# Kernel optimization log

Hardware: AMD Instinct MI355X
Metric: run time of the kernel (lower is better)

Reference implementation:

```python
import jax, jax.numpy as jnp
import numpy as np

TEMPERATURE = 8.0  # sqrt(head_dim=64)
_MASKING_VALUE = -1e30  # float32 branch of the original module


def setup_inputs() -> dict:
    key = jax.random.key(0)
    kq, kk, kv = jax.random.split(key, 3)
    B, H, S, D = 2, 12, 2048, 64
    q = jax.random.normal(kq, (B, H, S, D), dtype=jnp.float32)
    k = jax.random.normal(kk, (B, H, S, D), dtype=jnp.float32)
    v = jax.random.normal(kv, (B, H, S, D), dtype=jnp.float32)
    # causal mask, broadcastable over batch and heads; mask==0 -> masked
    mask = jnp.tril(jnp.ones((S, S), dtype=jnp.bool_))[None, None, :, :]
    return {"q": q, "k": k, "v": v, "mask": mask}


def reference(q, k, v, mask):
    # attn = (q / temperature) @ k^T  -> [B,H,S,S]
    scores = jnp.einsum("bhqd,bhkd->bhqk", q / TEMPERATURE, k)
    scores = jnp.where(mask, scores, _MASKING_VALUE)
    attn = jax.nn.softmax(scores, axis=-1)  # dropout in eval mode (identity)
    output = jnp.einsum("bhqk,bhkd->bhqd", attn, v)
    return (output, attn)
```

## Files before the change

kernel.cpp:

```cpp
#include <hip/hip_runtime.h>
#include <hip/hip_bf16.h>
#include <stdint.h>

#define SS 2048
#define DD 64
#define NHEAD 24
#define TQ 64
#define TK 64
#define NKT 32

typedef __attribute__((ext_vector_type(8))) short short8;
typedef __attribute__((ext_vector_type(4))) short short4v;
typedef __attribute__((ext_vector_type(4))) float f32x4;

#define QSCALE 0.18033688011112042f
#define MLOG   46.166241308446828f

#if __has_builtin(__builtin_amdgcn_exp2f)
#define EXP2(x) __builtin_amdgcn_exp2f(x)
#else
#define EXP2(x) exp2f(x)
#endif

__device__ __forceinline__ unsigned short f2bf(float x) {
  union { float f; unsigned u; } a; a.f = x;
  unsigned r = a.u + 0x7FFFu + ((a.u >> 16) & 1u);
  return (unsigned short)(r >> 16);
}
__device__ __forceinline__ float bf2f(unsigned short u) {
  union { unsigned u; float f; } a; a.u = ((unsigned)u) << 16;
  return a.f;
}

__device__ __forceinline__ void stage16(const unsigned char* g, unsigned char* l) {
  __builtin_amdgcn_global_load_lds(
      (const __attribute__((address_space(1))) unsigned int*)g,
      (__attribute__((address_space(3))) unsigned int*)l, 16, 0, 0);
}

__global__ __launch_bounds__(256) void prep_kernel(
    const float* __restrict__ q, const float* __restrict__ k,
    const float* __restrict__ v, unsigned short* __restrict__ qb,
    unsigned char* __restrict__ kb, unsigned char* __restrict__ vtb) {
  const int head = blockIdx.x >> 5;
  const int t64 = blockIdx.x & 31;
  const int tid = threadIdx.x;
  const int c4 = tid & 15;
  const size_t inbase = ((size_t)head * SS + (size_t)t64 * 64) * DD;
  const f32x4* qsrc = (const f32x4*)(q + inbase);
  const f32x4* ksrc = (const f32x4*)(k + inbase);
  const f32x4* vsrc = (const f32x4*)(v + inbase);
  unsigned short* qdst = qb + inbase;
  unsigned char* ktile = kb + ((size_t)(head * NKT + t64) << 13);
  unsigned char* vtile = vtb + ((size_t)(head * NKT + t64) << 13);
#pragma unroll
  for (int j = 0; j < 4; ++j) {
    const int row = (tid >> 4) + 16 * j;
    f32x4 xq = qsrc[row * 16 + c4];
    short4v hq;
    hq.x = (short)f2bf(xq.x * QSCALE); hq.y = (short)f2bf(xq.y * QSCALE);
    hq.z = (short)f2bf(xq.z * QSCALE); hq.w = (short)f2bf(xq.w * QSCALE);
    *(short4v*)(qdst + row * 64 + c4 * 4) = hq;

    f32x4 xk = ksrc[row * 16 + c4];
    short4v hk;
    hk.x = (short)f2bf(xk.x); hk.y = (short)f2bf(xk.y);
    hk.z = (short)f2bf(xk.z); hk.w = (short)f2bf(xk.w);
    const int chunk = c4 >> 1, half = c4 & 1;
    *(short4v*)(ktile + row * 128 + ((chunk ^ (row & 7)) << 4) + half * 8) = hk;

    f32x4 xv = vsrc[row * 16 + c4];
    float vals[4] = {xv.x, xv.y, xv.z, xv.w};
#pragma unroll
    for (int e = 0; e < 4; ++e) {
      const int d = c4 * 4 + e;
      *(unsigned short*)(vtile + d * 128 + (((row >> 3) ^ (d & 7)) << 4) +
                         (row & 7) * 2) = f2bf(vals[e]);
    }
  }
}

__global__ __launch_bounds__(256) void sdpa_kernel(
    const unsigned short* __restrict__ qb, const unsigned char* __restrict__ kb,
    const unsigned char* __restrict__ vtb, float* __restrict__ out,
    float* __restrict__ attn) {
  __shared__ unsigned char lds[40960];

  const int bid = blockIdx.x;
  const int xcd = bid & 7;
  const int seq = bid >> 3;
  const int head = xcd * 3 + (seq >> 5);
  const int qt = seq & 31;
  const int q0 = qt * TQ;

  const int tid = threadIdx.x;
  const int w = tid >> 6;
  const int l = tid & 63;
  const int lhi = l >> 4;
  const int llo = l & 15;

  const unsigned short* qh = qb + (size_t)head * SS * DD;
  const unsigned char* kh = kb + ((size_t)(head * NKT) << 13);
  const unsigned char* vh = vtb + ((size_t)(head * NKT) << 13);
  float* oh = out + (size_t)head * SS * DD;
  float* ah = attn + (size_t)head * SS * SS;

  unsigned char* ldsP = lds + 32768;

  const int qrow_a = q0 + 16 * w + llo;
  short8 qf0 = *(const short8*)(qh + (size_t)qrow_a * DD + lhi * 8);
  short8 qf1 = *(const short8*)(qh + (size_t)qrow_a * DD + lhi * 8 + 32);

  float lsum[4] = {0.f, 0.f, 0.f, 0.f};

  int b = 0;
  stage16(kh + tid * 16, lds + tid * 16);
  stage16(kh + 4096 + tid * 16, lds + 4096 + tid * 16);
  __syncthreads();
  for (int kt = 0; kt <= qt; ++kt) {
    if (kt < qt) {
      const unsigned char* src = kh + ((size_t)(kt + 1) << 13);
      unsigned char* dst = lds + (b ^ 1) * 8192;
      stage16(src + tid * 16, dst + tid * 16);
      stage16(src + 4096 + tid * 16, dst + 4096 + tid * 16);
    }
    const unsigned char* kbuf = lds + b * 8192;
    f32x4 s[4];
#pragma unroll
    for (int c = 0; c < 4; ++c) {
      const int br = 16 * c + llo;
      short8 kf0 = *(const short8*)(kbuf + br * 128 + ((lhi ^ (br & 7)) << 4));
      short8 kf1 = *(const short8*)(kbuf + br * 128 + (((lhi + 4) ^ (br & 7)) << 4));
      f32x4 acc = {0.f, 0.f, 0.f, 0.f};
      acc = __builtin_amdgcn_mfma_f32_16x16x32_bf16(qf0, kf0, acc, 0, 0, 0);
      acc = __builtin_amdgcn_mfma_f32_16x16x32_bf16(qf1, kf1, acc, 0, 0, 0);
      s[c] = acc;
    }
    if (kt == qt) {
#pragma unroll
      for (int c = 0; c < 4; ++c)
#pragma unroll
        for (int r = 0; r < 4; ++r) {
          int qrow = 16 * w + 4 * lhi + r;
          int kcol = 16 * c + llo;
          if (kcol > qrow) s[c][r] = -INFINITY;
        }
    }
#pragma unroll
    for (int c = 0; c < 4; ++c)
#pragma unroll
      for (int r = 0; r < 4; ++r) lsum[r] += EXP2(s[c][r] - MLOG);
    __syncthreads();
    b ^= 1;
  }

  float linv[4];
#pragma unroll
  for (int r = 0; r < 4; ++r) {
    float ps = lsum[r];
    ps += __shfl_xor(ps, 1);
    ps += __shfl_xor(ps, 2);
    ps += __shfl_xor(ps, 4);
    ps += __shfl_xor(ps, 8);
    linv[r] = 1.0f / ps;
  }

  f32x4 o[4];
#pragma unroll
  for (int c = 0; c < 4; ++c) o[c] = (f32x4){0.f, 0.f, 0.f, 0.f};

  b = 0;
  stage16(kh + tid * 16, lds + tid * 16);
  stage16(kh + 4096 + tid * 16, lds + 4096 + tid * 16);
  stage16(vh + tid * 16, lds + 16384 + tid * 16);
  stage16(vh + 4096 + tid * 16, lds + 16384 + 4096 + tid * 16);
  __syncthreads();
  for (int kt = 0; kt <= qt; ++kt) {
    if (kt < qt) {
      const unsigned char* ksrc = kh + ((size_t)(kt + 1) << 13);
      const unsigned char* vsrc = vh + ((size_t)(kt + 1) << 13);
      unsigned char* kdst = lds + (b ^ 1) * 8192;
      unsigned char* vdst = lds + 16384 + (b ^ 1) * 8192;
      stage16(ksrc + tid * 16, kdst + tid * 16);
      stage16(ksrc + 4096 + tid * 16, kdst + 4096 + tid * 16);
      stage16(vsrc + tid * 16, vdst + tid * 16);
      stage16(vsrc + 4096 + tid * 16, vdst + 4096 + tid * 16);
    }
    const unsigned char* kbuf = lds + b * 8192;
    const unsigned char* vbuf = lds + 16384 + b * 8192;

    f32x4 s[4];
#pragma unroll
    for (int c = 0; c < 4; ++c) {
      const int br = 16 * c + llo;
      short8 kf0 = *(const short8*)(kbuf + br * 128 + ((lhi ^ (br & 7)) << 4));
      short8 kf1 = *(const short8*)(kbuf + br * 128 + (((lhi + 4) ^ (br & 7)) << 4));
      f32x4 acc = {0.f, 0.f, 0.f, 0.f};
      acc = __builtin_amdgcn_mfma_f32_16x16x32_bf16(qf0, kf0, acc, 0, 0, 0);
      acc = __builtin_amdgcn_mfma_f32_16x16x32_bf16(qf1, kf1, acc, 0, 0, 0);
      s[c] = acc;
    }
    if (kt == qt) {
#pragma unroll
      for (int c = 0; c < 4; ++c)
#pragma unroll
        for (int r = 0; r < 4; ++r) {
          int qrow = 16 * w + 4 * lhi + r;
          int kcol = 16 * c + llo;
          if (kcol > qrow) s[c][r] = -INFINITY;
        }
    }
#pragma unroll
    for (int c = 0; c < 4; ++c)
#pragma unroll
      for (int r = 0; r < 4; ++r) {
        float p = EXP2(s[c][r] - MLOG) * linv[r];
        const int qrow = 16 * w + 4 * lhi + r;
        const int kcol = 16 * c + llo;
        *(unsigned short*)(ldsP + qrow * 128 + (((kcol >> 3) ^ (qrow & 7)) << 4) +
                           (kcol & 7) * 2) = f2bf(p);
      }
    __syncthreads();

    const int k0 = kt * TK;
#pragma unroll
    for (int j = 0; j < 4; ++j) {
      const int row = (tid >> 4) + 16 * j;
      const int cg = tid & 15;
      short4v pv = *(const short4v*)(ldsP + row * 128 +
                                     (((cg >> 1) ^ (row & 7)) << 4) + (cg & 1) * 8);
      f32x4 fo;
      fo.x = bf2f((unsigned short)pv.x);
      fo.y = bf2f((unsigned short)pv.y);
      fo.z = bf2f((unsigned short)pv.z);
      fo.w = bf2f((unsigned short)pv.w);
      *(f32x4*)(ah + (size_t)(q0 + row) * SS + k0 + cg * 4) = fo;
    }

    {
      const int pr = 16 * w + llo;
      short8 pa0 = *(const short8*)(ldsP + pr * 128 + ((lhi ^ (pr & 7)) << 4));
      short8 pa1 = *(const short8*)(ldsP + pr * 128 + (((lhi + 4) ^ (pr & 7)) << 4));
#pragma unroll
      for (int c = 0; c < 4; ++c) {
        const int vr = 16 * c + llo;
        short8 vb0 = *(const short8*)(vbuf + vr * 128 + ((lhi ^ (vr & 7)) << 4));
        short8 vb1 = *(const short8*)(vbuf + vr * 128 + (((lhi + 4) ^ (vr & 7)) << 4));
        o[c] = __builtin_amdgcn_mfma_f32_16x16x32_bf16(pa0, vb0, o[c], 0, 0, 0);
        o[c] = __builtin_amdgcn_mfma_f32_16x16x32_bf16(pa1, vb1, o[c], 0, 0, 0);
      }
    }
    __syncthreads();
    b ^= 1;
  }

  {
    const int zc = (qt + 1) * TK;
#pragma unroll
    for (int j = 0; j < 4; ++j) {
      int row = q0 + 16 * w + 4 * j + lhi;
      f32x4* dst = (f32x4*)(ah + (size_t)row * SS);
      for (int c = (zc >> 2) + llo; c < (SS >> 2); c += 16)
        dst[c] = (f32x4){0.f, 0.f, 0.f, 0.f};
    }
  }

#pragma unroll
  for (int c = 0; c < 4; ++c)
#pragma unroll
    for (int r = 0; r < 4; ++r) {
      int qrow = q0 + 16 * w + 4 * lhi + r;
      oh[(size_t)qrow * DD + 16 * c + llo] = o[c][r];
    }
}

extern "C" void kernel_launch(void* const* d_in, const int* in_sizes, int n_in,
                              void* d_out, int out_size, void* d_ws, size_t ws_size,
                              hipStream_t stream) {
  const float* q = (const float*)d_in[0];
  const float* k = (const float*)d_in[1];
  const float* v = (const float*)d_in[2];
  float* out = (float*)d_out;
  float* attn = out + (size_t)NHEAD * SS * DD;

  const size_t QKV_BYTES = (size_t)NHEAD * SS * DD * 2;
  unsigned short* qb = (unsigned short*)d_ws;
  unsigned char* kb = (unsigned char*)d_ws + QKV_BYTES;
  unsigned char* vtb = kb + QKV_BYTES;

  prep_kernel<<<dim3(NHEAD * NKT), dim3(256), 0, stream>>>(q, k, v, qb, kb, vtb);
  sdpa_kernel<<<dim3(NHEAD * NKT), dim3(256), 0, stream>>>(qb, kb, vtb, out, attn);
}
```

Before: 481.0 us.

## Keep P in registers via transposed QK MFMA and bpermute instead of LDS round-trip

Computes S^T by swapping the MFMA operands, so each lane holds scores for one query row. The softmax row sum then needs only two cross-lane shuffles. P is packed to bf16 in registers and reshuffled into the A-operand layout with ds_bpermute, which removes the LDS P buffer and one __syncthreads per tile. Attention rows are written straight from registers with nontemporal stores, deferred by one iteration to overlap with compute. The cost is more VGPR pressure and bpermute traffic, plus stores that are less coalesced because each lane writes 16-byte chunks along its own row.

```diff
diff --git a/kernel.cpp b/kernel.cpp
--- a/kernel.cpp
+++ b/kernel.cpp
@@ -5,7 +5,6 @@
 #define SS 2048
 #define DD 64
 #define NHEAD 24
-#define TQ 64
 #define TK 64
 #define NKT 32
 
@@ -26,10 +25,6 @@
   union { float f; unsigned u; } a; a.f = x;
   unsigned r = a.u + 0x7FFFu + ((a.u >> 16) & 1u);
   return (unsigned short)(r >> 16);
-}
-__device__ __forceinline__ float bf2f(unsigned short u) {
-  union { unsigned u; float f; } a; a.u = ((unsigned)u) << 16;
-  return a.f;
 }
 
 __device__ __forceinline__ void stage16(const unsigned char* g, unsigned char* l) {
@@ -84,39 +79,37 @@
     const unsigned short* __restrict__ qb, const unsigned char* __restrict__ kb,
     const unsigned char* __restrict__ vtb, float* __restrict__ out,
     float* __restrict__ attn) {
-  __shared__ unsigned char lds[40960];
+  __shared__ unsigned char lds[32768];
 
   const int bid = blockIdx.x;
   const int xcd = bid & 7;
   const int seq = bid >> 3;
   const int head = xcd * 3 + (seq >> 5);
   const int qt = seq & 31;
-  const int q0 = qt * TQ;
+  const int q0 = qt * TK;
 
   const int tid = threadIdx.x;
   const int w = tid >> 6;
   const int l = tid & 63;
   const int lhi = l >> 4;
   const int llo = l & 15;
+  const int qrl = 16 * w + llo;
 
   const unsigned short* qh = qb + (size_t)head * SS * DD;
   const unsigned char* kh = kb + ((size_t)(head * NKT) << 13);
   const unsigned char* vh = vtb + ((size_t)(head * NKT) << 13);
   float* oh = out + (size_t)head * SS * DD;
   float* ah = attn + (size_t)head * SS * SS;
-
-  unsigned char* ldsP = lds + 32768;
-
-  const int qrow_a = q0 + 16 * w + llo;
-  short8 qf0 = *(const short8*)(qh + (size_t)qrow_a * DD + lhi * 8);
-  short8 qf1 = *(const short8*)(qh + (size_t)qrow_a * DD + lhi * 8 + 32);
-
-  float lsum[4] = {0.f, 0.f, 0.f, 0.f};
-
-  int b = 0;
+  float* ah_row = ah + (size_t)(q0 + qrl) * SS;
+
+  short8 qf0 = *(const short8*)(qh + (size_t)(q0 + qrl) * DD + lhi * 8);
+  short8 qf1 = *(const short8*)(qh + (size_t)(q0 + qrl) * DD + lhi * 8 + 32);
+
+  float lsum = 0.f;
   stage16(kh + tid * 16, lds + tid * 16);
   stage16(kh + 4096 + tid * 16, lds + 4096 + tid * 16);
   __syncthreads();
+  int b = 0;
   for (int kt = 0; kt <= qt; ++kt) {
     if (kt < qt) {
       const unsigned char* src = kh + ((size_t)(kt + 1) << 13);
@@ -125,49 +118,35 @@
       stage16(src + 4096 + tid * 16, dst + 4096 + tid * 16);
     }
     const unsigned char* kbuf = lds + b * 8192;
-    f32x4 s[4];
+    const bool diag = (kt == qt);
 #pragma unroll
     for (int c = 0; c < 4; ++c) {
       const int br = 16 * c + llo;
       short8 kf0 = *(const short8*)(kbuf + br * 128 + ((lhi ^ (br & 7)) << 4));
       short8 kf1 = *(const short8*)(kbuf + br * 128 + (((lhi + 4) ^ (br & 7)) << 4));
       f32x4 acc = {0.f, 0.f, 0.f, 0.f};
-      acc = __builtin_amdgcn_mfma_f32_16x16x32_bf16(qf0, kf0, acc, 0, 0, 0);
-      acc = __builtin_amdgcn_mfma_f32_16x16x32_bf16(qf1, kf1, acc, 0, 0, 0);
-      s[c] = acc;
-    }
-    if (kt == qt) {
-#pragma unroll
-      for (int c = 0; c < 4; ++c)
-#pragma unroll
-        for (int r = 0; r < 4; ++r) {
-          int qrow = 16 * w + 4 * lhi + r;
-          int kcol = 16 * c + llo;
-          if (kcol > qrow) s[c][r] = -INFINITY;
-        }
-    }
-#pragma unroll
-    for (int c = 0; c < 4; ++c)
-#pragma unroll
-      for (int r = 0; r < 4; ++r) lsum[r] += EXP2(s[c][r] - MLOG);
+      acc = __builtin_amdgcn_mfma_f32_16x16x32_bf16(kf0, qf0, acc, 0, 0, 0);
+      acc = __builtin_amdgcn_mfma_f32_16x16x32_bf16(kf1, qf1, acc, 0, 0, 0);
+#pragma unroll
+      for (int r = 0; r < 4; ++r) {
+        float sv = acc[r];
+        if (diag && (16 * c + 4 * lhi + r > qrl)) sv = -INFINITY;
+        lsum += EXP2(sv - MLOG);
+      }
+    }
     __syncthreads();
     b ^= 1;
   }
-
-  float linv[4];
-#pragma unroll
-  for (int r = 0; r < 4; ++r) {
-    float ps = lsum[r];
-    ps += __shfl_xor(ps, 1);
-    ps += __shfl_xor(ps, 2);
-    ps += __shfl_xor(ps, 4);
-    ps += __shfl_xor(ps, 8);
-    linv[r] = 1.0f / ps;
-  }
+  lsum += __shfl_xor(lsum, 16);
+  lsum += __shfl_xor(lsum, 32);
+  const float linv = 1.0f / lsum;
 
   f32x4 o[4];
 #pragma unroll
   for (int c = 0; c < 4; ++c) o[c] = (f32x4){0.f, 0.f, 0.f, 0.f};
+
+  unsigned sv[8];
+  int k0p = 0;
 
   b = 0;
   stage16(kh + tid * 16, lds + tid * 16);
@@ -175,7 +154,22 @@
   stage16(vh + tid * 16, lds + 16384 + tid * 16);
   stage16(vh + 4096 + tid * 16, lds + 16384 + 4096 + tid * 16);
   __syncthreads();
+
+  const int i0 = ((((2 * lhi)) & 3) * 16 + llo) * 4;
+  const int i1 = ((((2 * lhi) + 1) & 3) * 16 + llo) * 4;
+
   for (int kt = 0; kt <= qt; ++kt) {
+    if (kt > 0) {
+#pragma unroll
+      for (int c = 0; c < 4; ++c) {
+        f32x4 fo;
+        fo.x = __uint_as_float(sv[2 * c] << 16);
+        fo.y = __uint_as_float(sv[2 * c] & 0xFFFF0000u);
+        fo.z = __uint_as_float(sv[2 * c + 1] << 16);
+        fo.w = __uint_as_float(sv[2 * c + 1] & 0xFFFF0000u);
+        __builtin_nontemporal_store(fo, (f32x4*)(ah_row + k0p + 16 * c + 4 * lhi));
+      }
+    }
     if (kt < qt) {
       const unsigned char* ksrc = kh + ((size_t)(kt + 1) << 13);
       const unsigned char* vsrc = vh + ((size_t)(kt + 1) << 13);
@@ -188,70 +182,68 @@
     }
     const unsigned char* kbuf = lds + b * 8192;
     const unsigned char* vbuf = lds + 16384 + b * 8192;
-
-    f32x4 s[4];
+    const bool diag = (kt == qt);
+
+    unsigned pk[8];
 #pragma unroll
     for (int c = 0; c < 4; ++c) {
       const int br = 16 * c + llo;
       short8 kf0 = *(const short8*)(kbuf + br * 128 + ((lhi ^ (br & 7)) << 4));
       short8 kf1 = *(const short8*)(kbuf + br * 128 + (((lhi + 4) ^ (br & 7)) << 4));
       f32x4 acc = {0.f, 0.f, 0.f, 0.f};
-      acc = __builtin_amdgcn_mfma_f32_16x16x32_bf16(qf0, kf0, acc, 0, 0, 0);
-      acc = __builtin_amdgcn_mfma_f32_16x16x32_bf16(qf1, kf1, acc, 0, 0, 0);
-      s[c] = acc;
-    }
-    if (kt == qt) {
-#pragma unroll
-      for (int c = 0; c < 4; ++c)
-#pragma unroll
-        for (int r = 0; r < 4; ++r) {
-          int qrow = 16 * w + 4 * lhi + r;
-          int kcol = 16 * c + llo;
-          if (kcol > qrow) s[c][r] = -INFINITY;
-        }
-    }
-#pragma unroll
-    for (int c = 0; c < 4; ++c)
+      acc = __builtin_amdgcn_mfma_f32_16x16x32_bf16(kf0, qf0, acc, 0, 0, 0);
+      acc = __builtin_amdgcn_mfma_f32_16x16x32_bf16(kf1, qf1, acc, 0, 0, 0);
+      float p[4];
 #pragma unroll
       for (int r = 0; r < 4; ++r) {
-        float p = EXP2(s[c][r] - MLOG) * linv[r];
-        const int qrow = 16 * w + 4 * lhi + r;
-        const int kcol = 16 * c + llo;
-        *(unsigned short*)(ldsP + qrow * 128 + (((kcol >> 3) ^ (qrow & 7)) << 4) +
-                           (kcol & 7) * 2) = f2bf(p);
+        float s = acc[r];
+        if (diag && (16 * c + 4 * lhi + r > qrl)) s = -INFINITY;
+        p[r] = EXP2(s - MLOG) * linv;
       }
-    __syncthreads();
-
-    const int k0 = kt * TK;
-#pragma unroll
-    for (int j = 0; j < 4; ++j) {
-      const int row = (tid >> 4) + 16 * j;
-      const int cg = tid & 15;
-      short4v pv = *(const short4v*)(ldsP + row * 128 +
-                                     (((cg >> 1) ^ (row & 7)) << 4) + (cg & 1) * 8);
-      f32x4 fo;
-      fo.x = bf2f((unsigned short)pv.x);
-      fo.y = bf2f((unsigned short)pv.y);
-      fo.z = bf2f((unsigned short)pv.z);
-      fo.w = bf2f((unsigned short)pv.w);
-      *(f32x4*)(ah + (size_t)(q0 + row) * SS + k0 + cg * 4) = fo;
-    }
-
-    {
-      const int pr = 16 * w + llo;
-      short8 pa0 = *(const short8*)(ldsP + pr * 128 + ((lhi ^ (pr & 7)) << 4));
-      short8 pa1 = *(const short8*)(ldsP + pr * 128 + (((lhi + 4) ^ (pr & 7)) << 4));
-#pragma unroll
-      for (int c = 0; c < 4; ++c) {
-        const int vr = 16 * c + llo;
-        short8 vb0 = *(const short8*)(vbuf + vr * 128 + ((lhi ^ (vr & 7)) << 4));
-        short8 vb1 = *(const short8*)(vbuf + vr * 128 + (((lhi + 4) ^ (vr & 7)) << 4));
-        o[c] = __builtin_amdgcn_mfma_f32_16x16x32_bf16(pa0, vb0, o[c], 0, 0, 0);
-        o[c] = __builtin_amdgcn_mfma_f32_16x16x32_bf16(pa1, vb1, o[c], 0, 0, 0);
-      }
-    }
+      pk[2 * c] = ((unsigned)f2bf(p[1]) << 16) | f2bf(p[0]);
+      pk[2 * c + 1] = ((unsigned)f2bf(p[3]) << 16) | f2bf(p[2]);
+    }
+
+    union U { int i[4]; short8 v; } fa0, fa1;
+#pragma unroll
+    for (int jb = 0; jb < 2; ++jb) {
+      int a0 = __builtin_amdgcn_ds_bpermute(i0, (int)pk[0 + jb]);
+      int b0 = __builtin_amdgcn_ds_bpermute(i0, (int)pk[2 + jb]);
+      fa0.i[jb] = (lhi < 2) ? a0 : b0;
+      int a1 = __builtin_amdgcn_ds_bpermute(i1, (int)pk[0 + jb]);
+      int b1 = __builtin_amdgcn_ds_bpermute(i1, (int)pk[2 + jb]);
+      fa0.i[2 + jb] = (lhi < 2) ? a1 : b1;
+      int c0 = __builtin_amdgcn_ds_bpermute(i0, (int)pk[4 + jb]);
+      int d0 = __builtin_amdgcn_ds_bpermute(i0, (int)pk[6 + jb]);
+      fa1.i[jb] = (lhi < 2) ? c0 : d0;
+      int c1 = __builtin_amdgcn_ds_bpermute(i1, (int)pk[4 + jb]);
+      int d1 = __builtin_amdgcn_ds_bpermute(i1, (int)pk[6 + jb]);
+      fa1.i[2 + jb] = (lhi < 2) ? c1 : d1;
+    }
+
+#pragma unroll
+    for (int c = 0; c < 4; ++c) {
+      const int vr = 16 * c + llo;
+      short8 vb0 = *(const short8*)(vbuf + vr * 128 + ((lhi ^ (vr & 7)) << 4));
+      short8 vb1 = *(const short8*)(vbuf + vr * 128 + (((lhi + 4) ^ (vr & 7)) << 4));
+      o[c] = __builtin_amdgcn_mfma_f32_16x16x32_bf16(fa0.v, vb0, o[c], 0, 0, 0);
+      o[c] = __builtin_amdgcn_mfma_f32_16x16x32_bf16(fa1.v, vb1, o[c], 0, 0, 0);
+    }
+
+#pragma unroll
+    for (int t = 0; t < 8; ++t) sv[t] = pk[t];
+    k0p = kt * TK;
     __syncthreads();
     b ^= 1;
+  }
+#pragma unroll
+  for (int c = 0; c < 4; ++c) {
+    f32x4 fo;
+    fo.x = __uint_as_float(sv[2 * c] << 16);
+    fo.y = __uint_as_float(sv[2 * c] & 0xFFFF0000u);
+    fo.z = __uint_as_float(sv[2 * c + 1] << 16);
+    fo.w = __uint_as_float(sv[2 * c + 1] & 0xFFFF0000u);
+    __builtin_nontemporal_store(fo, (f32x4*)(ah_row + k0p + 16 * c + 4 * lhi));
   }
 
   {
@@ -260,8 +252,9 @@
     for (int j = 0; j < 4; ++j) {
       int row = q0 + 16 * w + 4 * j + lhi;
       f32x4* dst = (f32x4*)(ah + (size_t)row * SS);
+      f32x4 z = {0.f, 0.f, 0.f, 0.f};
       for (int c = (zc >> 2) + llo; c < (SS >> 2); c += 16)
-        dst[c] = (f32x4){0.f, 0.f, 0.f, 0.f};
+        __builtin_nontemporal_store(z, dst + c);
     }
   }
 
```

New measurement: 516.5 us. +7.4%, slower.
